# Kernel tuning notes

Measured on AMD Instinct MI355X. Metric: run time of the kernel, lower is better.

## Reference

```python
import jax, jax.numpy as jnp
import numpy as np

N, E = 50000, 800000
F_IN, HID, CLS, K = 128, 128, 40, 4


def setup_inputs() -> dict:
    key = jax.random.key(0)
    ks = jax.random.split(key, 6)
    x = jax.random.normal(ks[0], (N, F_IN), jnp.float32)
    edge_src = jax.random.randint(ks[1], (E,), 0, N, jnp.int32)
    edge_dst = jax.random.randint(ks[2], (E,), 0, N, jnp.int32)
    glorot = lambda k, sh, fan: jax.random.normal(k, sh, jnp.float32) * np.float32(1.0 / np.sqrt(fan))
    W0 = glorot(ks[3], (K, F_IN, HID), F_IN)
    W1 = glorot(ks[4], (K, HID, HID), HID)
    W2 = glorot(ks[5], (K, HID, CLS), HID)
    b0 = jnp.zeros((HID,), jnp.float32)
    b1 = jnp.zeros((HID,), jnp.float32)
    b2 = jnp.zeros((CLS,), jnp.float32)
    return dict(x=x, edge_src=edge_src, edge_dst=edge_dst,
                W0=W0, b0=b0, W1=W1, b1=b1, W2=W2, b2=b2)


def _cheb_edge_norm(edge_src, edge_dst, n):
    # PyG ChebConv 'sym' norm with lambda_max=2: scaled Laplacian
    # L_hat = 2L/lambda_max - I = -D^{-1/2} A D^{-1/2}  (diagonal is exactly 0)
    ones = jnp.ones(edge_src.shape[0], jnp.float32)
    deg = jax.ops.segment_sum(ones, edge_src, num_segments=n)
    dinv = jnp.where(deg > 0, jax.lax.rsqrt(jnp.maximum(deg, 1.0)), 0.0)
    return -dinv[edge_src] * dinv[edge_dst]  # [E]


def _cheb_conv(x, edge_src, edge_dst, w_norm, W, b, n):
    # Chebyshev recurrence: Tx0 = x, Tx1 = L_hat x, Tx_k = 2 L_hat Tx_{k-1} - Tx_{k-2}
    def lhat(t):  # SpMM: out[dst] += w * t[src]
        return jax.ops.segment_sum(t[edge_src] * w_norm[:, None], edge_dst, num_segments=n)

    Tx0 = x
    out = Tx0 @ W[0]
    Tx1 = lhat(Tx0)
    out = out + Tx1 @ W[1]
    for k in range(2, W.shape[0]):
        Tx2 = 2.0 * lhat(Tx1) - Tx0
        out = out + Tx2 @ W[k]
        Tx0, Tx1 = Tx1, Tx2
    return out + b


def reference(x, edge_src, edge_dst, W0, b0, W1, b1, W2, b2):
    n = x.shape[0]
    w_norm = _cheb_edge_norm(edge_src, edge_dst, n)
    h = x
    x1 = h
    for W, b in ((W0, b0), (W1, b1), (W2, b2)):
        x1 = _cheb_conv(h, edge_src, edge_dst, w_norm, W, b, n)
        h = jax.nn.relu(x1)  # dropout(p=0.6) is identity in eval mode
    # original returns log_softmax of the LAST conv's pre-activation x1
    return jax.nn.log_softmax(x1, axis=1)
```

## Files before the change

kernel.cpp:

```cpp
#include <hip/hip_runtime.h>
#include <math.h>

#define NN 50000
#define NE 800000
#define FDIM 128
#define CLS 40
#define AW 512
#define ZW 256

#define BSH 7
#define BINS 128
#define NBUK 391
#define NB_E 196
#define EUNITS 1024
#define U4 (NE / 4)
#define HL (NBUK * NB_E)
#define HL2 (2 * HL)
#define SCAN_CHUNK 2048
#define NB_S ((HL2 + SCAN_CHUNK - 1) / SCAN_CHUNK)
#define BSLACK 4096

typedef __attribute__((ext_vector_type(8))) short short8v;
typedef __attribute__((ext_vector_type(8))) unsigned short ushort8v;
typedef __attribute__((ext_vector_type(4))) float f32x4;

__device__ inline float b2f(unsigned short u) {
    union { unsigned int i; float f; } v; v.i = ((unsigned)u) << 16; return v.f;
}
__device__ inline unsigned short f2b(float f) {
    unsigned int x = __float_as_uint(f);
    unsigned int r = (x + 0x7fffu + ((x >> 16) & 1u)) >> 16;
    return (unsigned short)r;
}

#define NB_CVT  3125
#define NB_WH   256
#define NB_WZ   128

__global__ __launch_bounds__(256) void prep_k(
        const int4* __restrict__ esrc4, const int4* __restrict__ edst4,
        int* __restrict__ hist,
        const float* __restrict__ x, unsigned short* __restrict__ Ab,
        const float* __restrict__ W0, const float* __restrict__ W1,
        const float* __restrict__ W2,
        unsigned short* __restrict__ Wt0, unsigned short* __restrict__ Wt1,
        unsigned short* __restrict__ Wz) {
    int b = blockIdx.x;
    int tid = threadIdx.x;
    if (b < NB_E) {
        __shared__ int lcd[NBUK], lcs[NBUK];
        for (int i = tid; i < NBUK; i += 256) { lcd[i] = 0; lcs[i] = 0; }
        __syncthreads();
        #pragma unroll
        for (int it = 0; it < 4; it++) {
            int u = b * EUNITS + it * 256 + tid;
            if (u < U4) {
                int4 s = esrc4[u], d = edst4[u];
                atomicAdd(&lcd[d.x >> BSH], 1); atomicAdd(&lcd[d.y >> BSH], 1);
                atomicAdd(&lcd[d.z >> BSH], 1); atomicAdd(&lcd[d.w >> BSH], 1);
                atomicAdd(&lcs[s.x >> BSH], 1); atomicAdd(&lcs[s.y >> BSH], 1);
                atomicAdd(&lcs[s.z >> BSH], 1); atomicAdd(&lcs[s.w >> BSH], 1);
            }
        }
        __syncthreads();
        for (int i = tid; i < NBUK; i += 256) {
            hist[i * NB_E + b] = lcd[i];
            hist[HL + i * NB_E + b] = lcs[i];
        }
    } else if (b < NB_E + NB_CVT) {
        int i = (b - NB_E) * 256 + tid;
        int row = i >> 4, cg = i & 15;
        const float4* xp = (const float4*)(x + (size_t)row * FDIM + cg * 8);
        float4 v0 = xp[0], v1 = xp[1];
        ushort8v r;
        r[0] = f2b(v0.x); r[1] = f2b(v0.y); r[2] = f2b(v0.z); r[3] = f2b(v0.w);
        r[4] = f2b(v1.x); r[5] = f2b(v1.y); r[6] = f2b(v1.z); r[7] = f2b(v1.w);
        *(ushort8v*)(Ab + (size_t)row * AW + cg * 8) = r;
    } else if (b < NB_E + NB_CVT + 2 * NB_WH) {
        int wi = b - NB_E - NB_CVT;
        const float* W = (wi < NB_WH) ? W0 : W1;
        unsigned short* Wfm = (wi < NB_WH) ? Wt0 : Wt1;
        int i = (wi % NB_WH) * 256 + tid;
        int j = i & 7, l = (i >> 3) & 63, kcl = (i >> 9) & 3, nt = (i >> 11) & 7, c = i >> 14;
        int r = kcl * 32 + (l >> 4) * 8 + j;
        int col = nt * 16 + (l & 15);
        Wfm[i] = f2b(W[((size_t)c * 128 + r) * 128 + col]);
    } else {
        int i = (b - NB_E - NB_CVT - 2 * NB_WH) * 256 + tid;
        int j = i & 7, l = (i >> 3) & 63, kcl = (i >> 9) & 3, nt = (i >> 11) & 7, half = (i >> 14) & 1;
        int k = kcl * 32 + (l >> 4) * 8 + j;
        int col = half * 128 + nt * 16 + (l & 15);
        int kcheb = col >> 6, cc = col & 63;
        float v = (cc < CLS) ? W2[((size_t)kcheb * 128 + k) * CLS + cc] : 0.0f;
        Wz[i] = f2b(v);
    }
}


__global__ void scanA_k(const int* __restrict__ hist, int* __restrict__ bsum) {
    __shared__ int lds[256];
    int base = blockIdx.x * SCAN_CHUNK;
    int s = 0;
    for (int j = threadIdx.x; j < SCAN_CHUNK; j += 256) {
        int i = base + j;
        if (i < HL2) s += hist[i];
    }
    lds[threadIdx.x] = s;
    __syncthreads();
    for (int off = 128; off > 0; off >>= 1) {
        if (threadIdx.x < off) lds[threadIdx.x] += lds[threadIdx.x + off];
        __syncthreads();
    }
    if (threadIdx.x == 0) bsum[blockIdx.x] = lds[0];
}

__global__ void scanB_k(int* bsum, int* scanned) {
    if (threadIdx.x == 0 && blockIdx.x == 0) {
        int run = 0;
        for (int b = 0; b < NB_S; b++) { int t = bsum[b]; bsum[b] = run; run += t; }
        scanned[HL2] = run;
    }
}

__global__ void scanC_k(const int* __restrict__ hist, const int* __restrict__ bsum,
                        int* __restrict__ scanned) {
    __shared__ int lds[256];
    int base = blockIdx.x * SCAN_CHUNK + threadIdx.x * 8;
    int v[8];
    int s = 0;
    #pragma unroll
    for (int j = 0; j < 8; j++) {
        int i = base + j;
        v[j] = (i < HL2) ? hist[i] : 0;
        s += v[j];
    }
    lds[threadIdx.x] = s;
    __syncthreads();
    for (int off = 1; off < 256; off <<= 1) {
        int t = (threadIdx.x >= (unsigned)off) ? lds[threadIdx.x - off] : 0;
        __syncthreads();
        lds[threadIdx.x] += t;
        __syncthreads();
    }
    int incl = lds[threadIdx.x];
    int excl = incl - s;
    int run = bsum[blockIdx.x] + excl;
    #pragma unroll
    for (int j = 0; j < 8; j++) {
        int i = base + j;
        if (i < HL2) scanned[i] = run;
        run += v[j];
    }
}


__global__ __launch_bounds__(256) void part_k(const int4* __restrict__ esrc4,
                                              const int4* __restrict__ edst4,
                                              const int* __restrict__ scanned,
                                              int* __restrict__ ebuf,
                                              unsigned short* __restrict__ sbuf) {
    __shared__ int lcd[NBUK], lcs[NBUK];
    int b = blockIdx.x;
    int tid = threadIdx.x;
    for (int i = tid; i < NBUK; i += 256) { lcd[i] = 0; lcs[i] = 0; }
    __syncthreads();
    #pragma unroll
    for (int it = 0; it < 4; it++) {
        int u = b * EUNITS + it * 256 + tid;
        if (u < U4) {
            int4 s = esrc4[u], d = edst4[u];
            int dd[4] = {d.x, d.y, d.z, d.w};
            int ss[4] = {s.x, s.y, s.z, s.w};
            #pragma unroll
            for (int j = 0; j < 4; j++) {
                int bin = dd[j] >> BSH;
                int r = atomicAdd(&lcd[bin], 1);
                ebuf[scanned[bin * NB_E + b] + r] = ((dd[j] & (BINS - 1)) << 16) | ss[j];
                int sbin = ss[j] >> BSH;
                int r2 = atomicAdd(&lcs[sbin], 1);
                sbuf[scanned[HL + sbin * NB_E + b] + r2 - NE] = (unsigned short)(ss[j] & (BINS - 1));
            }
        }
    }
}


__global__ __launch_bounds__(256) void degcnt_k(const int* __restrict__ scanned,
                                                const unsigned short* __restrict__ sbuf,
                                                float* __restrict__ dinv) {
    __shared__ int cnt[BINS];
    int b = blockIdx.x;
    int tid = threadIdx.x;
    int s0 = scanned[HL + b * NB_E] - NE;
    int s1 = scanned[HL + (b + 1) * NB_E] - NE;
    if (tid < BINS) cnt[tid] = 0;
    __syncthreads();
    for (int e = s0 + tid; e < s1; e += 256)
        atomicAdd(&cnt[sbuf[e]], 1);
    __syncthreads();
    if (tid < BINS) {
        int node = b * BINS + tid;
        if (node < NN) {
            int d = cnt[tid];
            dinv[node] = (d > 0) ? rsqrtf((float)d) : 0.0f;
        }
    }
    if (b == 0 && tid == 255) dinv[NN] = 0.0f;
}


__global__ __launch_bounds__(256) void bsort_k(const int* __restrict__ scanned,
                                               const int* __restrict__ ebuf,
                                               int* __restrict__ ews,
                                               int* __restrict__ rp,
                                               int* __restrict__ rpe) {
    __shared__ int cnt[BINS], excl[BINS], rnk[BINS];
    int b = blockIdx.x;
    int tid = threadIdx.x;
    int s0b = scanned[b * NB_E];
    int s1b = scanned[(b + 1) * NB_E];
    if (tid < BINS) { cnt[tid] = 0; rnk[tid] = 0; }
    __syncthreads();
    for (int e = s0b + tid; e < s1b; e += 256)
        atomicAdd(&cnt[ebuf[e] >> 16], 1);
    __syncthreads();
    if (tid == 0) {
        int run = 0;
        for (int i = 0; i < BINS; i++) { excl[i] = run; run += (cnt[i] + 31) & ~31; }
    }
    __syncthreads();
    int abase = (s0b + b * BSLACK + 31) & ~31;
    if (tid < BINS) {
        int node = b * BINS + tid;
        if (node < NN) {
            rp[node]  = abase + excl[tid];
            rpe[node] = abase + excl[tid] + ((cnt[tid] + 31) & ~31);
        }
    }
    for (int e = s0b + tid; e < s1b; e += 256) {
        int pk = ebuf[e];
        int low = pk >> 16;
        int pos = abase + excl[low] + atomicAdd(&rnk[low], 1);
        ews[pos] = pk & 0xFFFF;
    }
    for (int i = tid; i < BINS * 32; i += 256) {
        int bin = i >> 5;
        int off = cnt[bin] + (i & 31);
        if (off < ((cnt[bin] + 31) & ~31))
            ews[abase + excl[bin] + off] = NN;
    }
}


template <bool CHEB>
__global__ __launch_bounds__(256) void spmm_k(const unsigned short* __restrict__ inp,
                                              const unsigned short* __restrict__ prevp,
                                              unsigned short* __restrict__ outp,
                                              const int* __restrict__ rp,
                                              const int* __restrict__ rpe,
                                              const int* __restrict__ ews,
                                              const float* __restrict__ dinv) {
    int row = blockIdx.x * 4 + (threadIdx.x >> 6);
    int lane = threadIdx.x & 63;
    int slot = lane >> 4, ln = lane & 15;
    int e0 = rp[row], e1 = rpe[row];
    float dvr = dinv[row];
    float acc[8] = {0.f, 0.f, 0.f, 0.f, 0.f, 0.f, 0.f, 0.f};
    for (int e = e0; e < e1; e += 16) {
        int4 s4 = *(const int4*)&ews[e + slot * 4];
        ushort8v t0 = *(const ushort8v*)(inp + (size_t)s4.x * AW + ln * 8);
        ushort8v t1 = *(const ushort8v*)(inp + (size_t)s4.y * AW + ln * 8);
        ushort8v t2 = *(const ushort8v*)(inp + (size_t)s4.z * AW + ln * 8);
        ushort8v t3 = *(const ushort8v*)(inp + (size_t)s4.w * AW + ln * 8);
        float w0 = -dinv[s4.x] * dvr, w1 = -dinv[s4.y] * dvr;
        float w2 = -dinv[s4.z] * dvr, w3 = -dinv[s4.w] * dvr;
        #pragma unroll
        for (int j = 0; j < 8; j++)
            acc[j] += w0 * b2f(t0[j]) + w1 * b2f(t1[j]) + w2 * b2f(t2[j]) + w3 * b2f(t3[j]);
    }
    #pragma unroll
    for (int j = 0; j < 8; j++) {
        acc[j] += __shfl_xor(acc[j], 16);
        acc[j] += __shfl_xor(acc[j], 32);
    }
    if (slot == 0) {
        ushort8v r;
        if (CHEB) {
            ushort8v p = *(const ushort8v*)(prevp + (size_t)row * AW + ln * 8);
            #pragma unroll
            for (int j = 0; j < 8; j++) r[j] = f2b(2.f * acc[j] - b2f(p[j]));
        } else {
            #pragma unroll
            for (int j = 0; j < 8; j++) r[j] = f2b(acc[j]);
        }
        *(ushort8v*)(outp + (size_t)row * AW + ln * 8) = r;
    }
}


template <int MODE>
__global__ __launch_bounds__(256) void spmm64_k(const unsigned short* __restrict__ gsrc,
                                                const unsigned short* __restrict__ zadd,
                                                const unsigned short* __restrict__ bsub,
                                                unsigned short* __restrict__ wout,
                                                float* __restrict__ fout,
                                                const int* __restrict__ rp,
                                                const int* __restrict__ rpe,
                                                const int* __restrict__ ews,
                                                const float* __restrict__ dinv) {
    constexpr float SC = (MODE == 2) ? 1.0f : 2.0f;
    int row = blockIdx.x * 4 + (threadIdx.x >> 6);
    int lane = threadIdx.x & 63;
    int slot = lane >> 3, ln = lane & 7;
    int e0 = rp[row], e1 = rpe[row];
    float dvr = dinv[row];
    float acc[8] = {0.f, 0.f, 0.f, 0.f, 0.f, 0.f, 0.f, 0.f};
    for (int e = e0; e < e1; e += 32) {
        int4 s4 = *(const int4*)&ews[e + slot * 4];
        ushort8v t0 = *(const ushort8v*)(gsrc + (size_t)s4.x * 64 + ln * 8);
        ushort8v t1 = *(const ushort8v*)(gsrc + (size_t)s4.y * 64 + ln * 8);
        ushort8v t2 = *(const ushort8v*)(gsrc + (size_t)s4.z * 64 + ln * 8);
        ushort8v t3 = *(const ushort8v*)(gsrc + (size_t)s4.w * 64 + ln * 8);
        float w0 = -dinv[s4.x] * dvr, w1 = -dinv[s4.y] * dvr;
        float w2 = -dinv[s4.z] * dvr, w3 = -dinv[s4.w] * dvr;
        #pragma unroll
        for (int j = 0; j < 8; j++)
            acc[j] += w0 * b2f(t0[j]) + w1 * b2f(t1[j]) + w2 * b2f(t2[j]) + w3 * b2f(t3[j]);
    }
    #pragma unroll
    for (int j = 0; j < 8; j++) {
        acc[j] += __shfl_xor(acc[j], 8);
        acc[j] += __shfl_xor(acc[j], 16);
        acc[j] += __shfl_xor(acc[j], 32);
    }
    if (slot != 0) return;
    ushort8v zv = *(const ushort8v*)(zadd + (size_t)row * ZW + ln * 8);
    float v[8];
    if (MODE == 0) {
        #pragma unroll
        for (int j = 0; j < 8; j++) v[j] = b2f(zv[j]) + SC * acc[j];
    } else {
        constexpr int BS = (MODE == 1) ? ZW : 64;
        ushort8v bv = *(const ushort8v*)(bsub + (size_t)row * BS + ln * 8);
        #pragma unroll
        for (int j = 0; j < 8; j++) v[j] = b2f(zv[j]) + SC * acc[j] - b2f(bv[j]);
    }
    if (MODE < 2) {
        ushort8v r;
        #pragma unroll
        for (int j = 0; j < 8; j++) r[j] = f2b(v[j]);
        *(ushort8v*)(wout + (size_t)row * 64 + ln * 8) = r;
    } else {
        float m = -INFINITY;
        #pragma unroll
        for (int j = 0; j < 8; j++) if (ln * 8 + j < CLS) m = fmaxf(m, v[j]);
        #pragma unroll
        for (int off = 4; off >= 1; off >>= 1) m = fmaxf(m, __shfl_xor(m, off));
        float s = 0.f;
        #pragma unroll
        for (int j = 0; j < 8; j++) if (ln * 8 + j < CLS) s += __expf(v[j] - m);
        #pragma unroll
        for (int off = 4; off >= 1; off >>= 1) s += __shfl_xor(s, off);
        float ls = logf(s) + m;
        #pragma unroll
        for (int j = 0; j < 8; j++) {
            int col = ln * 8 + j;
            if (col < CLS) fout[(size_t)row * CLS + col] = v[j] - ls;
        }
    }
}


__global__ __launch_bounds__(256) void gemm_hid_k(const unsigned short* __restrict__ A,
                                                  const unsigned short* __restrict__ Wfm,
                                                  const float* __restrict__ bias,
                                                  unsigned short* __restrict__ Hout) {
    __shared__ unsigned short Blds[16384];
    int tid = threadIdx.x;
    int w = tid >> 6, lane = tid & 63, ln = lane & 15, gp = lane >> 4;
    int rowbase = blockIdx.x * 64 + w * 16;
    int rowc = rowbase + ln;
    if (rowc >= NN) rowc = NN - 1;
    const unsigned short* Arow = A + (size_t)rowc * AW + gp * 8;

    f32x4 acc[8];
    #pragma unroll
    for (int i = 0; i < 8; i++) acc[i] = (f32x4){0.f, 0.f, 0.f, 0.f};

    short8v acur[4], anxt[4];
    #pragma unroll
    for (int kcl = 0; kcl < 4; kcl++) acur[kcl] = *(const short8v*)(Arow + kcl * 32);
    {
        const ushort8v* g = (const ushort8v*)Wfm;
        ushort8v* s = (ushort8v*)Blds;
        #pragma unroll
        for (int i = 0; i < 8; i++) s[tid + i * 256] = g[tid + i * 256];
    }
    __syncthreads();

    for (int c = 0; c < 4; c++) {
        if (c < 3) {
            #pragma unroll
            for (int kcl = 0; kcl < 4; kcl++)
                anxt[kcl] = *(const short8v*)(Arow + (c + 1) * 128 + kcl * 32);
        }
        #pragma unroll
        for (int kcl = 0; kcl < 4; kcl++) {
            #pragma unroll
            for (int nt = 0; nt < 8; nt++) {
                short8v b = *(const short8v*)&Blds[((nt * 4 + kcl) * 64 + lane) * 8];
                acc[nt] = __builtin_amdgcn_mfma_f32_16x16x32_bf16(acur[kcl], b, acc[nt], 0, 0, 0);
            }
        }
        if (c < 3) {
            __syncthreads();
            const ushort8v* g = (const ushort8v*)(Wfm + (c + 1) * 16384);
            ushort8v* s = (ushort8v*)Blds;
            #pragma unroll
            for (int i = 0; i < 8; i++) s[tid + i * 256] = g[tid + i * 256];
            __syncthreads();
            #pragma unroll
            for (int kcl = 0; kcl < 4; kcl++) acur[kcl] = anxt[kcl];
        }
    }

    if (rowbase < NN) {
        #pragma unroll
        for (int nt = 0; nt < 8; nt++) {
            int col = nt * 16 + ln;
            float bv = bias[col];
            #pragma unroll
            for (int j = 0; j < 4; j++) {
                int r = rowbase + gp * 4 + j;
                Hout[(size_t)r * AW + col] = f2b(fmaxf(acc[nt][j] + bv, 0.0f));
            }
        }
    }
}


__global__ __launch_bounds__(256) void gemm_z_k(const unsigned short* __restrict__ A,
                                                const unsigned short* __restrict__ Wz,
                                                const float* __restrict__ b2,
                                                unsigned short* __restrict__ Z,
                                                unsigned short* __restrict__ B3c) {
    __shared__ unsigned short Blds[16384];
    int tid = threadIdx.x;
    int w = tid >> 6, lane = tid & 63, ln = lane & 15, gp = lane >> 4;
    int rowbase = blockIdx.x * 64 + w * 16;
    int rowc = rowbase + ln;
    if (rowc >= NN) rowc = NN - 1;
    const unsigned short* Arow = A + (size_t)rowc * AW + gp * 8;

    short8v af[4];
    #pragma unroll
    for (int kcl = 0; kcl < 4; kcl++) af[kcl] = *(const short8v*)(Arow + kcl * 32);

    for (int half = 0; half < 2; half++) {
        if (half) __syncthreads();
        {
            const ushort8v* g = (const ushort8v*)(Wz + half * 16384);
            ushort8v* s = (ushort8v*)Blds;
            #pragma unroll
            for (int i = 0; i < 8; i++) s[tid + i * 256] = g[tid + i * 256];
        }
        __syncthreads();
        f32x4 acc[8];
        #pragma unroll
        for (int i = 0; i < 8; i++) acc[i] = (f32x4){0.f, 0.f, 0.f, 0.f};
        #pragma unroll
        for (int kcl = 0; kcl < 4; kcl++) {
            #pragma unroll
            for (int nt = 0; nt < 8; nt++) {
                short8v b = *(const short8v*)&Blds[((nt * 4 + kcl) * 64 + lane) * 8];
                acc[nt] = __builtin_amdgcn_mfma_f32_16x16x32_bf16(af[kcl], b, acc[nt], 0, 0, 0);
            }
        }
        if (rowbase < NN) {
            #pragma unroll
            for (int nt = 0; nt < 8; nt++) {
                int col = half * 128 + nt * 16 + ln;
                float bv = (col < CLS) ? b2[col] : 0.0f;
                #pragma unroll
                for (int j = 0; j < 4; j++) {
                    int r = rowbase + gp * 4 + j;
                    unsigned short hv = f2b(acc[nt][j] + bv);
                    Z[(size_t)r * ZW + col] = hv;
                    if (half == 1 && nt >= 4) B3c[(size_t)r * 64 + (col - 192)] = hv;
                }
            }
        }
    }
}


extern "C" void kernel_launch(void* const* d_in, const int* in_sizes, int n_in,
                              void* d_out, int out_size, void* d_ws, size_t ws_size,
                              hipStream_t stream) {
    const float* x    = (const float*)d_in[0];
    const int*   esrc = (const int*)d_in[1];
    const int*   edst = (const int*)d_in[2];
    const float* W0   = (const float*)d_in[3];
    const float* b0   = (const float*)d_in[4];
    const float* W1   = (const float*)d_in[5];
    const float* b1   = (const float*)d_in[6];
    const float* W2   = (const float*)d_in[7];
    const float* b2   = (const float*)d_in[8];
    float* out = (float*)d_out;

    char* p = (char*)d_ws;
    auto alloc = [&](size_t bytes) -> void* {
        void* r = (void*)p;
        p += (bytes + 255) & ~(size_t)255;
        return r;
    };
    unsigned short* Abuf = (unsigned short*)alloc((size_t)(NN + 1) * AW * 2);
    unsigned short* Zbuf = (unsigned short*)alloc((size_t)NN * ZW * 2);
    unsigned short* B1b  = (unsigned short*)alloc((size_t)(NN + 1) * 64 * 2);
    unsigned short* B2b  = (unsigned short*)alloc((size_t)(NN + 1) * 64 * 2);
    unsigned short* B3b  = (unsigned short*)alloc((size_t)(NN + 1) * 64 * 2);
    int*   ews     = (int*)alloc((size_t)(NE + NBUK * BSLACK + 64) * 4);
    int*   ebuf    = (int*)alloc((size_t)NE * 4);
    unsigned short* sbuf = (unsigned short*)alloc((size_t)NE * 2);
    int*   hist    = (int*)alloc((size_t)HL2 * 4);
    int*   scanned = (int*)alloc((size_t)(HL2 + 1) * 4);
    int*   bsum    = (int*)alloc(NB_S * 4);
    unsigned short* Wt0 = (unsigned short*)alloc((size_t)128 * AW * 2);
    unsigned short* Wt1 = (unsigned short*)alloc((size_t)128 * AW * 2);
    unsigned short* Wz  = (unsigned short*)alloc((size_t)32768 * 2);
    int*   rp   = (int*)alloc(NN * 4);
    int*   rpe  = (int*)alloc(NN * 4);
    float* dinv = (float*)alloc((NN + 1) * 4);

    const int TB = 256;

    prep_k<<<NB_E + NB_CVT + 2 * NB_WH + NB_WZ, TB, 0, stream>>>(
        (const int4*)esrc, (const int4*)edst, hist,
        x, Abuf, W0, W1, W2, Wt0, Wt1, Wz);
    scanA_k<<<NB_S, TB, 0, stream>>>(hist, bsum);
    scanB_k<<<1, 64, 0, stream>>>(bsum, scanned);
    scanC_k<<<NB_S, TB, 0, stream>>>(hist, bsum, scanned);
    part_k<<<NB_E, TB, 0, stream>>>((const int4*)esrc, (const int4*)edst, scanned, ebuf, sbuf);
    degcnt_k<<<NBUK, TB, 0, stream>>>(scanned, sbuf, dinv);
    bsort_k<<<NBUK, TB, 0, stream>>>(scanned, ebuf, ews, rp, rpe);

    int gSpmm = (NN + 3) / 4;
    int gGemm = (NN + 63) / 64;

    unsigned short* s0 = Abuf + 0 * 128;
    unsigned short* s1 = Abuf + 1 * 128;
    unsigned short* s2 = Abuf + 2 * 128;
    unsigned short* s3 = Abuf + 3 * 128;

    for (int l = 0; l < 2; l++) {
        spmm_k<false><<<gSpmm, TB, 0, stream>>>(s0, nullptr, s1, rp, rpe, ews, dinv);
        spmm_k<true><<<gSpmm, TB, 0, stream>>>(s1, s0, s2, rp, rpe, ews, dinv);
        spmm_k<true><<<gSpmm, TB, 0, stream>>>(s2, s1, s3, rp, rpe, ews, dinv);
        const unsigned short* Wt = (l == 0) ? Wt0 : Wt1;
        const float* bl = (l == 0) ? b0 : b1;
        gemm_hid_k<<<gGemm, TB, 0, stream>>>(Abuf, Wt, bl, Abuf);
    }

    gemm_z_k<<<gGemm, TB, 0, stream>>>(Abuf, Wz, b2, Zbuf, B3b);
    spmm64_k<0><<<gSpmm, TB, 0, stream>>>(B3b, Zbuf + 128, nullptr,
                                          B2b, nullptr, rp, rpe, ews, dinv);
    spmm64_k<1><<<gSpmm, TB, 0, stream>>>(B2b, Zbuf + 64, Zbuf + 192,
                                          B1b, nullptr, rp, rpe, ews, dinv);
    spmm64_k<2><<<gSpmm, TB, 0, stream>>>(B1b, Zbuf, B2b,
                                          nullptr, out, rp, rpe, ews, dinv);
}
```

Before: 366.2 us.

## Quantize SpMM gather operands to int8 with per-row scales folded into dinv

The gathered feature rows used by the Chebyshev SpMM kernels are stored as int8 with a per-row scale instead of bf16, and the scale is folded into the edge normalisation factor. Each producing SpMM now also writes a quantized copy of its output, and an extra hquant kernel quantizes the rows after each GEMM. This halves the bytes fetched in the random row gathers, which dominate the SpMM cost. In exchange it adds extra quantize passes and writes, and int8 precision loss may push results past tolerance.

```diff
diff --git a/kernel.cpp b/kernel.cpp
--- a/kernel.cpp
+++ b/kernel.cpp
@@ -31,6 +31,17 @@
     unsigned int x = __float_as_uint(f);
     unsigned int r = (x + 0x7fffu + ((x >> 16) & 1u)) >> 16;
     return (unsigned short)r;
+}
+__device__ inline float sb(int w, int j) {
+    return (float)((w << (24 - 8 * j)) >> 24);
+}
+__device__ inline int2 qpack(const float* f, float scale) {
+    int2 r; r.x = 0; r.y = 0;
+    #pragma unroll
+    for (int j = 0; j < 4; j++) r.x |= (((int)rintf(f[j] * scale)) & 0xff) << (8 * j);
+    #pragma unroll
+    for (int j = 0; j < 4; j++) r.y |= (((int)rintf(f[4 + j] * scale)) & 0xff) << (8 * j);
+    return r;
 }
 
 #define NB_CVT  3125
@@ -187,7 +198,8 @@
 
 __global__ __launch_bounds__(256) void degcnt_k(const int* __restrict__ scanned,
                                                 const unsigned short* __restrict__ sbuf,
-                                                float* __restrict__ dinv) {
+                                                float* __restrict__ dinv,
+                                                float* __restrict__ dqall) {
     __shared__ int cnt[BINS];
     int b = blockIdx.x;
     int tid = threadIdx.x;
@@ -205,7 +217,10 @@
             dinv[node] = (d > 0) ? rsqrtf((float)d) : 0.0f;
         }
     }
-    if (b == 0 && tid == 255) dinv[NN] = 0.0f;
+    if (b == 0) {
+        if (tid < 7) dqall[tid * (NN + 1) + NN] = 0.0f;
+        if (tid == 255) dinv[NN] = 0.0f;
+    }
 }
 
 
@@ -252,10 +267,35 @@
 }
 
 
+template <int NL, int STRIDE>
+__global__ __launch_bounds__(256) void hquant_k(const unsigned short* __restrict__ src,
+                                                const float* __restrict__ dinv,
+                                                signed char* __restrict__ Q,
+                                                float* __restrict__ dqout) {
+    int i = blockIdx.x * 256 + threadIdx.x;
+    int row = i / NL, ln = i % NL;
+    if (row >= NN) return;
+    ushort8v u = *(const ushort8v*)(src + (size_t)row * STRIDE + ln * 8);
+    float f[8];
+    float m = 0.0f;
+    #pragma unroll
+    for (int j = 0; j < 8; j++) { f[j] = b2f(u[j]); m = fmaxf(m, fabsf(f[j])); }
+    #pragma unroll
+    for (int off = 1; off < NL; off <<= 1) m = fmaxf(m, __shfl_xor(m, off));
+    float scale = (m > 0.0f) ? 127.0f / m : 0.0f;
+    int2 q = qpack(f, scale);
+    *(int2*)(Q + (size_t)row * (NL * 8) + ln * 8) = q;
+    if (ln == 0) dqout[row] = dinv[row] * m * (1.0f / 127.0f);
+}
+
+
 template <bool CHEB>
-__global__ __launch_bounds__(256) void spmm_k(const unsigned short* __restrict__ inp,
+__global__ __launch_bounds__(256) void spmm_k(const signed char* __restrict__ Qin,
+                                              const float* __restrict__ dqin,
                                               const unsigned short* __restrict__ prevp,
                                               unsigned short* __restrict__ outp,
+                                              signed char* __restrict__ Qout,
+                                              float* __restrict__ dqout,
                                               const int* __restrict__ rp,
                                               const int* __restrict__ rpe,
                                               const int* __restrict__ ews,
@@ -268,15 +308,17 @@
     float acc[8] = {0.f, 0.f, 0.f, 0.f, 0.f, 0.f, 0.f, 0.f};
     for (int e = e0; e < e1; e += 16) {
         int4 s4 = *(const int4*)&ews[e + slot * 4];
-        ushort8v t0 = *(const ushort8v*)(inp + (size_t)s4.x * AW + ln * 8);
-        ushort8v t1 = *(const ushort8v*)(inp + (size_t)s4.y * AW + ln * 8);
-        ushort8v t2 = *(const ushort8v*)(inp + (size_t)s4.z * AW + ln * 8);
-        ushort8v t3 = *(const ushort8v*)(inp + (size_t)s4.w * AW + ln * 8);
-        float w0 = -dinv[s4.x] * dvr, w1 = -dinv[s4.y] * dvr;
-        float w2 = -dinv[s4.z] * dvr, w3 = -dinv[s4.w] * dvr;
-        #pragma unroll
-        for (int j = 0; j < 8; j++)
-            acc[j] += w0 * b2f(t0[j]) + w1 * b2f(t1[j]) + w2 * b2f(t2[j]) + w3 * b2f(t3[j]);
+        int2 t0 = *(const int2*)(Qin + (size_t)s4.x * 128 + ln * 8);
+        int2 t1 = *(const int2*)(Qin + (size_t)s4.y * 128 + ln * 8);
+        int2 t2 = *(const int2*)(Qin + (size_t)s4.z * 128 + ln * 8);
+        int2 t3 = *(const int2*)(Qin + (size_t)s4.w * 128 + ln * 8);
+        float w0 = -dqin[s4.x] * dvr, w1 = -dqin[s4.y] * dvr;
+        float w2 = -dqin[s4.z] * dvr, w3 = -dqin[s4.w] * dvr;
+        #pragma unroll
+        for (int j = 0; j < 4; j++) {
+            acc[j]     += w0 * sb(t0.x, j) + w1 * sb(t1.x, j) + w2 * sb(t2.x, j) + w3 * sb(t3.x, j);
+            acc[4 + j] += w0 * sb(t0.y, j) + w1 * sb(t1.y, j) + w2 * sb(t2.y, j) + w3 * sb(t3.y, j);
+        }
     }
     #pragma unroll
     for (int j = 0; j < 8; j++) {
@@ -284,25 +326,38 @@
         acc[j] += __shfl_xor(acc[j], 32);
     }
     if (slot == 0) {
-        ushort8v r;
+        float r[8];
         if (CHEB) {
             ushort8v p = *(const ushort8v*)(prevp + (size_t)row * AW + ln * 8);
             #pragma unroll
-            for (int j = 0; j < 8; j++) r[j] = f2b(2.f * acc[j] - b2f(p[j]));
+            for (int j = 0; j < 8; j++) r[j] = 2.f * acc[j] - b2f(p[j]);
         } else {
             #pragma unroll
-            for (int j = 0; j < 8; j++) r[j] = f2b(acc[j]);
-        }
-        *(ushort8v*)(outp + (size_t)row * AW + ln * 8) = r;
+            for (int j = 0; j < 8; j++) r[j] = acc[j];
+        }
+        ushort8v o;
+        float m = 0.0f;
+        #pragma unroll
+        for (int j = 0; j < 8; j++) { o[j] = f2b(r[j]); m = fmaxf(m, fabsf(r[j])); }
+        *(ushort8v*)(outp + (size_t)row * AW + ln * 8) = o;
+        #pragma unroll
+        for (int off = 1; off < 16; off <<= 1) m = fmaxf(m, __shfl_xor(m, off));
+        float scale = (m > 0.0f) ? 127.0f / m : 0.0f;
+        int2 q = qpack(r, scale);
+        *(int2*)(Qout + (size_t)row * 128 + ln * 8) = q;
+        if (ln == 0) dqout[row] = dvr * m * (1.0f / 127.0f);
     }
 }
 
 
 template <int MODE>
-__global__ __launch_bounds__(256) void spmm64_k(const unsigned short* __restrict__ gsrc,
+__global__ __launch_bounds__(256) void spmm64_k(const signed char* __restrict__ Qin,
+                                                const float* __restrict__ dqin,
                                                 const unsigned short* __restrict__ zadd,
                                                 const unsigned short* __restrict__ bsub,
                                                 unsigned short* __restrict__ wout,
+                                                signed char* __restrict__ Qout,
+                                                float* __restrict__ dqout,
                                                 float* __restrict__ fout,
                                                 const int* __restrict__ rp,
                                                 const int* __restrict__ rpe,
@@ -317,15 +372,17 @@
     float acc[8] = {0.f, 0.f, 0.f, 0.f, 0.f, 0.f, 0.f, 0.f};
     for (int e = e0; e < e1; e += 32) {
         int4 s4 = *(const int4*)&ews[e + slot * 4];
-        ushort8v t0 = *(const ushort8v*)(gsrc + (size_t)s4.x * 64 + ln * 8);
-        ushort8v t1 = *(const ushort8v*)(gsrc + (size_t)s4.y * 64 + ln * 8);
-        ushort8v t2 = *(const ushort8v*)(gsrc + (size_t)s4.z * 64 + ln * 8);
-        ushort8v t3 = *(const ushort8v*)(gsrc + (size_t)s4.w * 64 + ln * 8);
-        float w0 = -dinv[s4.x] * dvr, w1 = -dinv[s4.y] * dvr;
-        float w2 = -dinv[s4.z] * dvr, w3 = -dinv[s4.w] * dvr;
-        #pragma unroll
-        for (int j = 0; j < 8; j++)
-            acc[j] += w0 * b2f(t0[j]) + w1 * b2f(t1[j]) + w2 * b2f(t2[j]) + w3 * b2f(t3[j]);
+        int2 t0 = *(const int2*)(Qin + (size_t)s4.x * 64 + ln * 8);
+        int2 t1 = *(const int2*)(Qin + (size_t)s4.y * 64 + ln * 8);
+        int2 t2 = *(const int2*)(Qin + (size_t)s4.z * 64 + ln * 8);
+        int2 t3 = *(const int2*)(Qin + (size_t)s4.w * 64 + ln * 8);
+        float w0 = -dqin[s4.x] * dvr, w1 = -dqin[s4.y] * dvr;
+        float w2 = -dqin[s4.z] * dvr, w3 = -dqin[s4.w] * dvr;
+        #pragma unroll
+        for (int j = 0; j < 4; j++) {
+            acc[j]     += w0 * sb(t0.x, j) + w1 * sb(t1.x, j) + w2 * sb(t2.x, j) + w3 * sb(t3.x, j);
+            acc[4 + j] += w0 * sb(t0.y, j) + w1 * sb(t1.y, j) + w2 * sb(t2.y, j) + w3 * sb(t3.y, j);
+        }
     }
     #pragma unroll
     for (int j = 0; j < 8; j++) {
@@ -347,9 +404,16 @@
     }
     if (MODE < 2) {
         ushort8v r;
-        #pragma unroll
-        for (int j = 0; j < 8; j++) r[j] = f2b(v[j]);
+        float m = 0.0f;
+        #pragma unroll
+        for (int j = 0; j < 8; j++) { r[j] = f2b(v[j]); m = fmaxf(m, fabsf(v[j])); }
         *(ushort8v*)(wout + (size_t)row * 64 + ln * 8) = r;
+        #pragma unroll
+        for (int off = 1; off < 8; off <<= 1) m = fmaxf(m, __shfl_xor(m, off));
+        float scale = (m > 0.0f) ? 127.0f / m : 0.0f;
+        int2 q = qpack(v, scale);
+        *(int2*)(Qout + (size_t)row * 64 + ln * 8) = q;
+        if (ln == 0) dqout[row] = dvr * m * (1.0f / 127.0f);
     } else {
         float m = -INFINITY;
         #pragma unroll
@@ -519,6 +583,9 @@
     unsigned short* B1b  = (unsigned short*)alloc((size_t)(NN + 1) * 64 * 2);
     unsigned short* B2b  = (unsigned short*)alloc((size_t)(NN + 1) * 64 * 2);
     unsigned short* B3b  = (unsigned short*)alloc((size_t)(NN + 1) * 64 * 2);
+    signed char* Qb = (signed char*)alloc((size_t)4 * (NN + 1) * 128);
+    signed char* Qc = (signed char*)alloc((size_t)3 * (NN + 1) * 64);
+    float* dqall = (float*)alloc((size_t)7 * (NN + 1) * 4);
     int*   ews     = (int*)alloc((size_t)(NE + NBUK * BSLACK + 64) * 4);
     int*   ebuf    = (int*)alloc((size_t)NE * 4);
     unsigned short* sbuf = (unsigned short*)alloc((size_t)NE * 2);
@@ -532,6 +599,21 @@
     int*   rpe  = (int*)alloc(NN * 4);
     float* dinv = (float*)alloc((NN + 1) * 4);
 
+    signed char* Q0 = Qb;
+    signed char* Q1 = Qb + (size_t)1 * (NN + 1) * 128;
+    signed char* Q2 = Qb + (size_t)2 * (NN + 1) * 128;
+    signed char* Q3 = Qb + (size_t)3 * (NN + 1) * 128;
+    signed char* Qc3 = Qc;
+    signed char* Qc2 = Qc + (size_t)1 * (NN + 1) * 64;
+    signed char* Qc1 = Qc + (size_t)2 * (NN + 1) * 64;
+    float* dq0 = dqall;
+    float* dq1 = dqall + 1 * (NN + 1);
+    float* dq2 = dqall + 2 * (NN + 1);
+    float* dq3 = dqall + 3 * (NN + 1);
+    float* dqc3 = dqall + 4 * (NN + 1);
+    float* dqc2 = dqall + 5 * (NN + 1);
+    float* dqc1 = dqall + 6 * (NN + 1);
+
     const int TB = 256;
 
     prep_k<<<NB_E + NB_CVT + 2 * NB_WH + NB_WZ, TB, 0, stream>>>(
@@ -541,31 +623,37 @@
     scanB_k<<<1, 64, 0, stream>>>(bsum, scanned);
     scanC_k<<<NB_S, TB, 0, stream>>>(hist, bsum, scanned);
     part_k<<<NB_E, TB, 0, stream>>>((const int4*)esrc, (const int4*)edst, scanned, ebuf, sbuf);
-    degcnt_k<<<NBUK, TB, 0, stream>>>(scanned, sbuf, dinv);
+    degcnt_k<<<NBUK, TB, 0, stream>>>(scanned, sbuf, dinv, dqall);
     bsort_k<<<NBUK, TB, 0, stream>>>(scanned, ebuf, ews, rp, rpe);
 
     int gSpmm = (NN + 3) / 4;
     int gGemm = (NN + 63) / 64;
+    int gHq128 = NN * 16 / TB;
+    int gHq64  = (NN * 8 + TB - 1) / TB;
 
     unsigned short* s0 = Abuf + 0 * 128;
     unsigned short* s1 = Abuf + 1 * 128;
     unsigned short* s2 = Abuf + 2 * 128;
     unsigned short* s3 = Abuf + 3 * 128;
 
+    hquant_k<16, AW><<<gHq128, TB, 0, stream>>>(s0, dinv, Q0, dq0);
+
     for (int l = 0; l < 2; l++) {
-        spmm_k<false><<<gSpmm, TB, 0, stream>>>(s0, nullptr, s1, rp, rpe, ews, dinv);
-        spmm_k<true><<<gSpmm, TB, 0, stream>>>(s1, s0, s2, rp, rpe, ews, dinv);
-        spmm_k<true><<<gSpmm, TB, 0, stream>>>(s2, s1, s3, rp, rpe, ews, dinv);
+        spmm_k<false><<<gSpmm, TB, 0, stream>>>(Q0, dq0, nullptr, s1, Q1, dq1, rp, rpe, ews, dinv);
+        spmm_k<true><<<gSpmm, TB, 0, stream>>>(Q1, dq1, s0, s2, Q2, dq2, rp, rpe, ews, dinv);
+        spmm_k<true><<<gSpmm, TB, 0, stream>>>(Q2, dq2, s1, s3, Q3, dq3, rp, rpe, ews, dinv);
         const unsigned short* Wt = (l == 0) ? Wt0 : Wt1;
         const float* bl = (l == 0) ? b0 : b1;
         gemm_hid_k<<<gGemm, TB, 0, stream>>>(Abuf, Wt, bl, Abuf);
+        hquant_k<16, AW><<<gHq128, TB, 0, stream>>>(s0, dinv, Q0, dq0);
     }
 
     gemm_z_k<<<gGemm, TB, 0, stream>>>(Abuf, Wz, b2, Zbuf, B3b);
-    spmm64_k<0><<<gSpmm, TB, 0, stream>>>(B3b, Zbuf + 128, nullptr,
-                                          B2b, nullptr, rp, rpe, ews, dinv);
-    spmm64_k<1><<<gSpmm, TB, 0, stream>>>(B2b, Zbuf + 64, Zbuf + 192,
-                                          B1b, nullptr, rp, rpe, ews, dinv);
-    spmm64_k<2><<<gSpmm, TB, 0, stream>>>(B1b, Zbuf, B2b,
-                                          nullptr, out, rp, rpe, ews, dinv);
-}
+    hquant_k<8, 64><<<gHq64, TB, 0, stream>>>(B3b, dinv, Qc3, dqc3);
+    spmm64_k<0><<<gSpmm, TB, 0, stream>>>(Qc3, dqc3, Zbuf + 128, nullptr,
+                                          B2b, Qc2, dqc2, nullptr, rp, rpe, ews, dinv);
+    spmm64_k<1><<<gSpmm, TB, 0, stream>>>(Qc2, dqc2, Zbuf + 64, Zbuf + 192,
+                                          B1b, Qc1, dqc1, nullptr, rp, rpe, ews, dinv);
+    spmm64_k<2><<<gSpmm, TB, 0, stream>>>(Qc1, dqc1, Zbuf, B2b,
+                                          nullptr, nullptr, nullptr, out, rp, rpe, ews, dinv);
+}
```

Result: slower. 389.3 us (+6.3%).
